# Performance work log

Hardware: AMD Instinct MI355X
Metric: run time of the kernel (lower is better)

Reference implementation:

```python
import jax, jax.numpy as jnp
import numpy as np

N, E, F, H, G, C = 50000, 600000, 128, 128, 500, 10
BN_EPS = 1e-5

def setup_inputs() -> dict:
    key = jax.random.key(0)
    ks = jax.random.split(key, 20)
    def lin(k, fan_in, shape):
        b = 1.0 / np.sqrt(fan_in)
        return jax.random.uniform(k, shape, jnp.float32, -b, b)
    inp = {
        'x': jax.random.normal(ks[0], (N, F), jnp.float32),
        'edge_index': jax.random.randint(ks[1], (2, E), 0, N, jnp.int64),
        'batch': jnp.sort(jax.random.randint(ks[2], (N,), 0, G, jnp.int64)),
        # conv1 MLP: Linear(F,H) -> BN(H) -> ReLU -> Dropout -> Linear(H,H) -> ReLU
        'W1a': lin(ks[3], F, (F, H)), 'b1a': lin(ks[4], F, (H,)),
        'g1': jnp.ones((H,), jnp.float32), 'be1': jnp.zeros((H,), jnp.float32),
        'm1': jnp.zeros((H,), jnp.float32), 'v1': jnp.ones((H,), jnp.float32),
        'W1b': lin(ks[5], H, (H, H)), 'b1b': lin(ks[6], H, (H,)),
        # conv2 MLP: Linear(H,H) -> ReLU -> BN(H) -> Dropout -> Linear(H,H) -> ReLU
        'W2a': lin(ks[7], H, (H, H)), 'b2a': lin(ks[8], H, (H,)),
        'g2': jnp.ones((H,), jnp.float32), 'be2': jnp.zeros((H,), jnp.float32),
        'm2': jnp.zeros((H,), jnp.float32), 'v2': jnp.ones((H,), jnp.float32),
        'W2b': lin(ks[9], H, (H, H)), 'b2b': lin(ks[10], H, (H,)),
        # heads
        'Wl1': lin(ks[11], 2 * H, (2 * H, H // 2)), 'bl1': lin(ks[12], 2 * H, (H // 2,)),
        'Wl2': lin(ks[13], H // 2, (H // 2, C)), 'bl2': lin(ks[14], H // 2, (C,)),
    }
    return inp

def _bn(h, g, b, m, v):
    return (h - m) * (g / jnp.sqrt(v + BN_EPS)) + b

def _gin_aggregate(x, src, dst):
    # out[i] = x[i] + sum_{j->i} x[j]  (GINConv with eps=0)
    return x + jax.ops.segment_sum(x[src], dst, num_segments=N)

def reference(x, edge_index, batch,
              W1a, b1a, g1, be1, m1, v1, W1b, b1b,
              W2a, b2a, g2, be2, m2, v2, W2b, b2b,
              Wl1, bl1, Wl2, bl2):
    src, dst = edge_index[0], edge_index[1]
    # conv1
    a1 = _gin_aggregate(x, src, dst)                       # [N, F]
    h1 = _bn(a1 @ W1a + b1a, g1, be1, m1, v1)
    h1 = jax.nn.relu(h1)                                   # dropout = identity (eval)
    h1 = jax.nn.relu(h1 @ W1b + b1b)                       # [N, H]
    # conv2
    a2 = _gin_aggregate(h1, src, dst)                      # [N, H]
    h2 = jax.nn.relu(a2 @ W2a + b2a)
    h2 = _bn(h2, g2, be2, m2, v2)
    h2 = jax.nn.relu(h2 @ W2b + b2b)                       # [N, H]
    # global add pool per graph
    p1 = jax.ops.segment_sum(h1, batch, num_segments=G)    # [G, H]
    p2 = jax.ops.segment_sum(h2, batch, num_segments=G)    # [G, H]
    z = jnp.concatenate((p1, p2), axis=1)                  # [G, 2H]
    z = jax.nn.relu(z @ Wl1 + bl1)
    return z @ Wl2 + bl2                                   # [G, C]
```

## Files before the change

kernel.cpp:

```cpp
#include <hip/hip_runtime.h>

#define N_NODES 50000
#define N_EDGES 600000
#define HDIM 128
#define NGRAPH 500
#define NCLASS 10
#define BN_EPS 1e-5f
#define KSLOT 64

typedef short short8 __attribute__((ext_vector_type(8)));
typedef float floatx4 __attribute__((ext_vector_type(4)));

__device__ __forceinline__ float bf2f(unsigned short u) {
    unsigned int v = ((unsigned int)u) << 16;
    return __uint_as_float(v);
}
__device__ __forceinline__ unsigned short f2bf(float f) {
    unsigned int u = __float_as_uint(f);
    unsigned int r = (u + 0x7fffu + ((u >> 16) & 1u)) >> 16;
    return (unsigned short)r;
}

#define NB_CAST 6250
#define NB_ZERO 196
#define NB_PREPW 256
#define NB_SETUP (NB_CAST + NB_ZERO + NB_PREPW + 1)

__global__ void k_setup(const float* __restrict__ x, unsigned short* __restrict__ xb,
                        int* __restrict__ cnt,
                        const float* __restrict__ W1a, const float* __restrict__ W1b,
                        const float* __restrict__ W2a, const float* __restrict__ W2b,
                        unsigned short* __restrict__ wpack,
                        const float* __restrict__ b1a, const float* __restrict__ g1,
                        const float* __restrict__ be1, const float* __restrict__ m1,
                        const float* __restrict__ v1, const float* __restrict__ b1b,
                        const float* __restrict__ b2a, const float* __restrict__ g2,
                        const float* __restrict__ be2, const float* __restrict__ m2,
                        const float* __restrict__ v2, const float* __restrict__ b2b,
                        float* __restrict__ ep) {
    int b = blockIdx.x;
    int t = threadIdx.x;
    if (b < NB_CAST) {
        int i = b * 256 + t;
        float4 v = ((const float4*)x)[i];
        ushort4 o;
        o.x = f2bf(v.x); o.y = f2bf(v.y); o.z = f2bf(v.z); o.w = f2bf(v.w);
        ((ushort4*)xb)[i] = o;
        return;
    }
    b -= NB_CAST;
    if (b < NB_ZERO) {
        int i = b * 256 + t;
        if (i < N_NODES) cnt[i] = 0;
        return;
    }
    b -= NB_ZERO;
    if (b < NB_PREPW) {
        int e = b * 256 + t;
        int w = e >> 14;
        int s_ = e & 16383;
        int j = s_ & 7;
        int m = (s_ >> 3) & 15;
        int q = (s_ >> 7) & 3;
        int ks = (s_ >> 9) & 3;
        int ct = (s_ >> 11) & 7;
        int n = ct * 16 + m;
        int k;
        float scale = 1.f;
        if (w == 0 || w == 2) {
            k = ks * 32 + q * 8 + j;
        } else {
            k = (ks * 2 + (j >> 2)) * 16 + q * 4 + (j & 3);
            if (w == 3) scale = g2[k] * rsqrtf(v2[k] + BN_EPS);
        }
        const float* W = (w == 0) ? W1a : (w == 1) ? W1b : (w == 2) ? W2a : W2b;
        wpack[e] = f2bf(W[k * 128 + n] * scale);
        return;
    }
    if (t < 128) {
        int j = t;
        float s1 = g1[j] * rsqrtf(v1[j] + BN_EPS);
        ep[0 * 256 + 0 + j]   = s1;
        ep[0 * 256 + 128 + j] = (b1a[j] - m1[j]) * s1 + be1[j];
        ep[1 * 256 + 0 + j]   = 1.f;
        ep[1 * 256 + 128 + j] = b2a[j];
        ep[512 + j] = b1b[j];
        float acc = b2b[j];
        for (int k = 0; k < 128; k++) {
            float s2k = g2[k] * rsqrtf(v2[k] + BN_EPS);
            acc += (be2[k] - m2[k] * s2k) * W2b[k * 128 + j];
        }
        ep[512 + 128 + j] = acc;
    }
}

__global__ void k_scatter(const int* __restrict__ src, const int* __restrict__ dst,
                          int* __restrict__ cnt, int* __restrict__ adj, int e) {
    int i = blockIdx.x * blockDim.x + threadIdx.x;
    if (i < e) {
        int d = dst[i];
        int p = atomicAdd(&cnt[d], 1);
        if (p < KSLOT) adj[d * KSLOT + p] = src[i];
    }
}

__global__ __launch_bounds__(256, 2) void k_conv(const unsigned short* __restrict__ A,
                                                 const int* __restrict__ cnt,
                                                 const int* __restrict__ adj,
                                                 const unsigned short* __restrict__ WaP,
                                                 const unsigned short* __restrict__ WbP,
                                                 const float* __restrict__ epi,
                                                 const float* __restrict__ epf,
                                                 unsigned short* __restrict__ Out, int n) {
    __shared__ unsigned short Wl[2][16384];
    int t = threadIdx.x;
    int lane = t & 63;
    int w = t >> 6;
    int q = lane >> 4;
    int m = lane & 15;

    int base = blockIdx.x * 128 + w * 32;

    #pragma unroll
    for (int i = 0; i < 8; i++) {
        int c = t + 256 * i;
        *(short8*)(Wl[0] + c * 8) = *(const short8*)(WaP + c * 8);
        *(short8*)(Wl[1] + c * 8) = *(const short8*)(WbP + c * 8);
    }

    short8 a1[2][4];
    #pragma unroll
    for (int rt = 0; rt < 2; rt++) {
        int node = base + rt * 16 + m;
        if (node >= n) node = n - 1;
        float acc[4][8];
        #pragma unroll
        for (int s = 0; s < 4; s++) {
            short8 sv = *(const short8*)(A + (size_t)node * 128 + s * 32 + q * 8);
            #pragma unroll
            for (int j = 0; j < 8; j++) acc[s][j] = bf2f((unsigned short)sv[j]);
        }
        int len = cnt[node];
        if (len > KSLOT) len = KSLOT;
        const int* ad = adj + node * KSLOT;
        int i = 0;
        for (; i + 4 <= len; i += 4) {
            int u0 = ad[i], u1 = ad[i + 1], u2 = ad[i + 2], u3 = ad[i + 3];
            short8 f0[4], f1[4], f2[4], f3[4];
            #pragma unroll
            for (int s = 0; s < 4; s++) {
                f0[s] = *(const short8*)(A + (size_t)u0 * 128 + s * 32 + q * 8);
                f1[s] = *(const short8*)(A + (size_t)u1 * 128 + s * 32 + q * 8);
                f2[s] = *(const short8*)(A + (size_t)u2 * 128 + s * 32 + q * 8);
                f3[s] = *(const short8*)(A + (size_t)u3 * 128 + s * 32 + q * 8);
            }
            #pragma unroll
            for (int s = 0; s < 4; s++)
                #pragma unroll
                for (int j = 0; j < 8; j++)
                    acc[s][j] += bf2f((unsigned short)f0[s][j]) + bf2f((unsigned short)f1[s][j]) +
                                 bf2f((unsigned short)f2[s][j]) + bf2f((unsigned short)f3[s][j]);
        }
        if (i + 2 <= len) {
            int u0 = ad[i], u1 = ad[i + 1];
            short8 f0[4], f1[4];
            #pragma unroll
            for (int s = 0; s < 4; s++) {
                f0[s] = *(const short8*)(A + (size_t)u0 * 128 + s * 32 + q * 8);
                f1[s] = *(const short8*)(A + (size_t)u1 * 128 + s * 32 + q * 8);
            }
            #pragma unroll
            for (int s = 0; s < 4; s++)
                #pragma unroll
                for (int j = 0; j < 8; j++)
                    acc[s][j] += bf2f((unsigned short)f0[s][j]) + bf2f((unsigned short)f1[s][j]);
            i += 2;
        }
        if (i < len) {
            int u0 = ad[i];
            #pragma unroll
            for (int s = 0; s < 4; s++) {
                short8 f0 = *(const short8*)(A + (size_t)u0 * 128 + s * 32 + q * 8);
                #pragma unroll
                for (int j = 0; j < 8; j++) acc[s][j] += bf2f((unsigned short)f0[j]);
            }
        }
        #pragma unroll
        for (int s = 0; s < 4; s++)
            #pragma unroll
            for (int j = 0; j < 8; j++) a1[rt][s][j] = (short)f2bf(acc[s][j]);
    }
    __syncthreads();

    int lbase = (q * 16 + m) * 8;

    floatx4 acc1[2][8];
    #pragma unroll
    for (int a = 0; a < 2; a++)
        #pragma unroll
        for (int c = 0; c < 8; c++) acc1[a][c] = (floatx4)0.f;
    #pragma unroll
    for (int s = 0; s < 4; s++) {
        #pragma unroll
        for (int ct = 0; ct < 8; ct++) {
            short8 wf = *(const short8*)(Wl[0] + (ct * 4 + s) * 512 + lbase);
            acc1[0][ct] = __builtin_amdgcn_mfma_f32_16x16x32_bf16(wf, a1[0][s], acc1[0][ct], 0, 0, 0);
            acc1[1][ct] = __builtin_amdgcn_mfma_f32_16x16x32_bf16(wf, a1[1][s], acc1[1][ct], 0, 0, 0);
        }
    }

    short8 a2[2][4];
    #pragma unroll
    for (int s = 0; s < 4; s++) {
        #pragma unroll
        for (int j = 0; j < 8; j++) {
            int ct = s * 2 + (j >> 2);
            int r = j & 3;
            int col = ct * 16 + q * 4 + r;
            float P = epi[col], Q = epi[128 + col];
            #pragma unroll
            for (int a = 0; a < 2; a++) {
                float v = fmaxf(fmaf(acc1[a][ct][r], P, Q), 0.f);
                a2[a][s][j] = (short)f2bf(v);
            }
        }
    }

    floatx4 acc2[2][8];
    #pragma unroll
    for (int a = 0; a < 2; a++)
        #pragma unroll
        for (int c = 0; c < 8; c++) acc2[a][c] = (floatx4)0.f;
    #pragma unroll
    for (int s = 0; s < 4; s++) {
        #pragma unroll
        for (int ct = 0; ct < 8; ct++) {
            short8 wf = *(const short8*)(Wl[1] + (ct * 4 + s) * 512 + lbase);
            acc2[0][ct] = __builtin_amdgcn_mfma_f32_16x16x32_bf16(a2[0][s], wf, acc2[0][ct], 0, 0, 0);
            acc2[1][ct] = __builtin_amdgcn_mfma_f32_16x16x32_bf16(a2[1][s], wf, acc2[1][ct], 0, 0, 0);
        }
    }

    #pragma unroll
    for (int ct = 0; ct < 8; ct++) {
        int col = ct * 16 + m;
        float Qf = epf[col];
        #pragma unroll
        for (int a = 0; a < 2; a++) {
            #pragma unroll
            for (int r = 0; r < 4; r++) {
                int gr = base + a * 16 + q * 4 + r;
                if (gr < n)
                    Out[(size_t)gr * 128 + col] = f2bf(fmaxf(acc2[a][ct][r] + Qf, 0.f));
            }
        }
    }
}

__global__ void k_pool_head(const unsigned short* __restrict__ h1, const unsigned short* __restrict__ h2,
                            const int* __restrict__ batch, const float* __restrict__ Wl1,
                            const float* __restrict__ bl1, const float* __restrict__ Wl2,
                            const float* __restrict__ bl2, float* __restrict__ out) {
    int g = blockIdx.x;
    int t = threadIdx.x;
    int lo = 0, hi = N_NODES;
    while (lo < hi) { int mid = (lo + hi) >> 1; if (batch[mid] < g) lo = mid + 1; else hi = mid; }
    int start = lo;
    lo = 0; hi = N_NODES;
    while (lo < hi) { int mid = (lo + hi) >> 1; if (batch[mid] < g + 1) lo = mid + 1; else hi = mid; }
    int end = lo;

    int w = t >> 6, l = t & 63;
    const unsigned int* h = (w < 2) ? (const unsigned int*)h1 : (const unsigned int*)h2;
    int sub = w & 1;
    float ax = 0.f, ay = 0.f;
    int i = start + sub;
    for (; i + 6 < end; i += 8) {
        unsigned int v0 = h[(size_t)(i + 0) * 64 + l];
        unsigned int v1 = h[(size_t)(i + 2) * 64 + l];
        unsigned int v2 = h[(size_t)(i + 4) * 64 + l];
        unsigned int v3 = h[(size_t)(i + 6) * 64 + l];
        ax += bf2f((unsigned short)(v0 & 0xffff)) + bf2f((unsigned short)(v1 & 0xffff)) +
              bf2f((unsigned short)(v2 & 0xffff)) + bf2f((unsigned short)(v3 & 0xffff));
        ay += bf2f((unsigned short)(v0 >> 16)) + bf2f((unsigned short)(v1 >> 16)) +
              bf2f((unsigned short)(v2 >> 16)) + bf2f((unsigned short)(v3 >> 16));
    }
    for (; i < end; i += 2) {
        unsigned int v0 = h[(size_t)i * 64 + l];
        ax += bf2f((unsigned short)(v0 & 0xffff));
        ay += bf2f((unsigned short)(v0 >> 16));
    }

    __shared__ float red[4][128];
    __shared__ float zin[256];
    __shared__ float zmid[64];
    red[w][2 * l] = ax;
    red[w][2 * l + 1] = ay;
    __syncthreads();
    int mat = t >> 7, col = t & 127;
    zin[t] = red[mat * 2][col] + red[mat * 2 + 1][col];
    __syncthreads();
    if (t < 64) {
        float acc = bl1[t];
        #pragma unroll 8
        for (int k = 0; k < 256; k++) acc = fmaf(zin[k], Wl1[k * 64 + t], acc);
        zmid[t] = fmaxf(acc, 0.f);
    }
    __syncthreads();
    if (t < NCLASS) {
        float acc = bl2[t];
        #pragma unroll
        for (int j = 0; j < 64; j++) acc = fmaf(zmid[j], Wl2[j * 10 + t], acc);
        out[g * NCLASS + t] = acc;
    }
}


extern "C" void kernel_launch(void* const* d_in, const int* in_sizes, int n_in,
                              void* d_out, int out_size, void* d_ws, size_t ws_size,
                              hipStream_t stream) {
    const float* x   = (const float*)d_in[0];
    const int* eidx  = (const int*)d_in[1];
    const int* batch = (const int*)d_in[2];
    const float* W1a = (const float*)d_in[3];
    const float* b1a = (const float*)d_in[4];
    const float* g1  = (const float*)d_in[5];
    const float* be1 = (const float*)d_in[6];
    const float* m1  = (const float*)d_in[7];
    const float* v1  = (const float*)d_in[8];
    const float* W1b = (const float*)d_in[9];
    const float* b1b = (const float*)d_in[10];
    const float* W2a = (const float*)d_in[11];
    const float* b2a = (const float*)d_in[12];
    const float* g2  = (const float*)d_in[13];
    const float* be2 = (const float*)d_in[14];
    const float* m2  = (const float*)d_in[15];
    const float* v2  = (const float*)d_in[16];
    const float* W2b = (const float*)d_in[17];
    const float* b2b = (const float*)d_in[18];
    const float* Wl1 = (const float*)d_in[19];
    const float* bl1 = (const float*)d_in[20];
    const float* Wl2 = (const float*)d_in[21];
    const float* bl2 = (const float*)d_in[22];
    const int* srcv = eidx;
    const int* dstv = eidx + N_EDGES;

    char* ws = (char*)d_ws;
    size_t off = 0;
    auto alloc = [&](size_t bytes) -> void* {
        void* p = ws + off;
        off = (off + bytes + 255) & ~(size_t)255;
        return p;
    };
    int* cnt      = (int*)alloc(sizeof(int) * N_NODES);
    int* adj      = (int*)alloc(sizeof(int) * (size_t)N_NODES * KSLOT);
    float* ep     = (float*)alloc(sizeof(float) * 768);
    unsigned short* wpack = (unsigned short*)alloc(sizeof(unsigned short) * 4 * 16384);
    unsigned short* xb    = (unsigned short*)alloc(sizeof(unsigned short) * (size_t)N_NODES * HDIM);
    unsigned short* bufB  = (unsigned short*)alloc(sizeof(unsigned short) * (size_t)N_NODES * HDIM);
    unsigned short* bufC  = (unsigned short*)alloc(sizeof(unsigned short) * (size_t)N_NODES * HDIM);
    (void)ws_size; (void)in_sizes; (void)n_in; (void)out_size;

    float* outp = (float*)d_out;

    k_setup<<<dim3(NB_SETUP), dim3(256), 0, stream>>>(
        x, xb, cnt, W1a, W1b, W2a, W2b, wpack,
        b1a, g1, be1, m1, v1, b1b, b2a, g2, be2, m2, v2, b2b, ep);
    k_scatter<<<dim3((N_EDGES + 255) / 256), dim3(256), 0, stream>>>(srcv, dstv, cnt, adj, N_EDGES);

    dim3 cgrid((N_NODES + 127) / 128), cblk(256);
    k_conv<<<cgrid, cblk, 0, stream>>>(xb, cnt, adj, wpack + 0 * 16384, wpack + 1 * 16384,
                                       ep + 0, ep + 512, bufC, N_NODES);
    k_conv<<<cgrid, cblk, 0, stream>>>(bufC, cnt, adj, wpack + 2 * 16384, wpack + 3 * 16384,
                                       ep + 256, ep + 640, bufB, N_NODES);
    k_pool_head<<<dim3(NGRAPH), dim3(256), 0, stream>>>(bufC, bufB, batch, Wl1, bl1, Wl2, bl2, outp);
}
```

Before: 270.4 us.

## Drop LDS weight staging and halve rows per wave in GIN conv kernel

Removes the 64KB shared-memory copy of both weight matrices and reads weight fragments directly from global memory (L2/L1 cached). Each wave now handles 16 nodes instead of 32, halving per-thread accumulator registers, and the block count doubles with launch bounds raised to allow 4 blocks per CU. The goal is more concurrent waves to hide the latency of the irregular neighbor gathers. The cost is repeated global weight loads per wave and less reuse of each weight fragment, since it now feeds one MFMA instead of two.

```diff
diff --git a/kernel.cpp b/kernel.cpp
--- a/kernel.cpp
+++ b/kernel.cpp
@@ -104,7 +104,7 @@
     }
 }
 
-__global__ __launch_bounds__(256, 2) void k_conv(const unsigned short* __restrict__ A,
+__global__ __launch_bounds__(256, 4) void k_conv(const unsigned short* __restrict__ A,
                                                  const int* __restrict__ cnt,
                                                  const int* __restrict__ adj,
                                                  const unsigned short* __restrict__ WaP,
@@ -112,34 +112,24 @@
                                                  const float* __restrict__ epi,
                                                  const float* __restrict__ epf,
                                                  unsigned short* __restrict__ Out, int n) {
-    __shared__ unsigned short Wl[2][16384];
     int t = threadIdx.x;
     int lane = t & 63;
     int w = t >> 6;
     int q = lane >> 4;
     int m = lane & 15;
 
-    int base = blockIdx.x * 128 + w * 32;
-
-    #pragma unroll
-    for (int i = 0; i < 8; i++) {
-        int c = t + 256 * i;
-        *(short8*)(Wl[0] + c * 8) = *(const short8*)(WaP + c * 8);
-        *(short8*)(Wl[1] + c * 8) = *(const short8*)(WbP + c * 8);
-    }
-
-    short8 a1[2][4];
-    #pragma unroll
-    for (int rt = 0; rt < 2; rt++) {
-        int node = base + rt * 16 + m;
-        if (node >= n) node = n - 1;
-        float acc[4][8];
-        #pragma unroll
-        for (int s = 0; s < 4; s++) {
-            short8 sv = *(const short8*)(A + (size_t)node * 128 + s * 32 + q * 8);
-            #pragma unroll
-            for (int j = 0; j < 8; j++) acc[s][j] = bf2f((unsigned short)sv[j]);
-        }
+    int base = blockIdx.x * 64 + w * 16;
+    int node = base + m;
+    if (node >= n) node = n - 1;
+
+    float acc[4][8];
+    #pragma unroll
+    for (int s = 0; s < 4; s++) {
+        short8 sv = *(const short8*)(A + (size_t)node * 128 + s * 32 + q * 8);
+        #pragma unroll
+        for (int j = 0; j < 8; j++) acc[s][j] = bf2f((unsigned short)sv[j]);
+    }
+    {
         int len = cnt[node];
         if (len > KSLOT) len = KSLOT;
         const int* ad = adj + node * KSLOT;
@@ -185,31 +175,28 @@
                 for (int j = 0; j < 8; j++) acc[s][j] += bf2f((unsigned short)f0[j]);
             }
         }
-        #pragma unroll
-        for (int s = 0; s < 4; s++)
-            #pragma unroll
-            for (int j = 0; j < 8; j++) a1[rt][s][j] = (short)f2bf(acc[s][j]);
-    }
-    __syncthreads();
-
-    int lbase = (q * 16 + m) * 8;
-
-    floatx4 acc1[2][8];
-    #pragma unroll
-    for (int a = 0; a < 2; a++)
-        #pragma unroll
-        for (int c = 0; c < 8; c++) acc1[a][c] = (floatx4)0.f;
+    }
+    short8 a1[4];
+    #pragma unroll
+    for (int s = 0; s < 4; s++)
+        #pragma unroll
+        for (int j = 0; j < 8; j++) a1[s][j] = (short)f2bf(acc[s][j]);
+
+    int lbase = lane * 8;
+
+    floatx4 acc1[8];
+    #pragma unroll
+    for (int c = 0; c < 8; c++) acc1[c] = (floatx4)0.f;
     #pragma unroll
     for (int s = 0; s < 4; s++) {
         #pragma unroll
         for (int ct = 0; ct < 8; ct++) {
-            short8 wf = *(const short8*)(Wl[0] + (ct * 4 + s) * 512 + lbase);
-            acc1[0][ct] = __builtin_amdgcn_mfma_f32_16x16x32_bf16(wf, a1[0][s], acc1[0][ct], 0, 0, 0);
-            acc1[1][ct] = __builtin_amdgcn_mfma_f32_16x16x32_bf16(wf, a1[1][s], acc1[1][ct], 0, 0, 0);
-        }
-    }
-
-    short8 a2[2][4];
+            short8 wf = *(const short8*)(WaP + (ct * 4 + s) * 512 + lbase);
+            acc1[ct] = __builtin_amdgcn_mfma_f32_16x16x32_bf16(wf, a1[s], acc1[ct], 0, 0, 0);
+        }
+    }
+
+    short8 a2[4];
     #pragma unroll
     for (int s = 0; s < 4; s++) {
         #pragma unroll
@@ -218,26 +205,20 @@
             int r = j & 3;
             int col = ct * 16 + q * 4 + r;
             float P = epi[col], Q = epi[128 + col];
-            #pragma unroll
-            for (int a = 0; a < 2; a++) {
-                float v = fmaxf(fmaf(acc1[a][ct][r], P, Q), 0.f);
-                a2[a][s][j] = (short)f2bf(v);
-            }
-        }
-    }
-
-    floatx4 acc2[2][8];
-    #pragma unroll
-    for (int a = 0; a < 2; a++)
-        #pragma unroll
-        for (int c = 0; c < 8; c++) acc2[a][c] = (floatx4)0.f;
+            float v = fmaxf(fmaf(acc1[ct][r], P, Q), 0.f);
+            a2[s][j] = (short)f2bf(v);
+        }
+    }
+
+    floatx4 acc2[8];
+    #pragma unroll
+    for (int c = 0; c < 8; c++) acc2[c] = (floatx4)0.f;
     #pragma unroll
     for (int s = 0; s < 4; s++) {
         #pragma unroll
         for (int ct = 0; ct < 8; ct++) {
-            short8 wf = *(const short8*)(Wl[1] + (ct * 4 + s) * 512 + lbase);
-            acc2[0][ct] = __builtin_amdgcn_mfma_f32_16x16x32_bf16(a2[0][s], wf, acc2[0][ct], 0, 0, 0);
-            acc2[1][ct] = __builtin_amdgcn_mfma_f32_16x16x32_bf16(a2[1][s], wf, acc2[1][ct], 0, 0, 0);
+            short8 wf = *(const short8*)(WbP + (ct * 4 + s) * 512 + lbase);
+            acc2[ct] = __builtin_amdgcn_mfma_f32_16x16x32_bf16(a2[s], wf, acc2[ct], 0, 0, 0);
         }
     }
 
@@ -246,13 +227,10 @@
         int col = ct * 16 + m;
         float Qf = epf[col];
         #pragma unroll
-        for (int a = 0; a < 2; a++) {
-            #pragma unroll
-            for (int r = 0; r < 4; r++) {
-                int gr = base + a * 16 + q * 4 + r;
-                if (gr < n)
-                    Out[(size_t)gr * 128 + col] = f2bf(fmaxf(acc2[a][ct][r] + Qf, 0.f));
-            }
+        for (int r = 0; r < 4; r++) {
+            int gr = base + q * 4 + r;
+            if (gr < n)
+                Out[(size_t)gr * 128 + col] = f2bf(fmaxf(acc2[ct][r] + Qf, 0.f));
         }
     }
 }
@@ -368,7 +346,7 @@
         b1a, g1, be1, m1, v1, b1b, b2a, g2, be2, m2, v2, b2b, ep);
     k_scatter<<<dim3((N_EDGES + 255) / 256), dim3(256), 0, stream>>>(srcv, dstv, cnt, adj, N_EDGES);
 
-    dim3 cgrid((N_NODES + 127) / 128), cblk(256);
+    dim3 cgrid((N_NODES + 63) / 64), cblk(256);
     k_conv<<<cgrid, cblk, 0, stream>>>(xb, cnt, adj, wpack + 0 * 16384, wpack + 1 * 16384,
                                        ep + 0, ep + 512, bufC, N_NODES);
     k_conv<<<cgrid, cblk, 0, stream>>>(bufC, cnt, adj, wpack + 2 * 16384, wpack + 3 * 16384,
```

New measurement: 264.1 us. -2.3%, faster.
